# Optimization experiments

Measured on AMD Instinct MI355X. Metric: run time of the kernel, lower is better.

## Reference

```python
import jax, jax.numpy as jnp
import numpy as np

EPS = 1e-12  # matches torch F.normalize eps


def _l2_normalize(x, axis):
    n = jnp.sqrt(jnp.sum(x * x, axis=axis, keepdims=True))
    return x / jnp.maximum(n, EPS)


def setup_inputs() -> dict:
    key = jax.random.key(0)
    k1, k2 = jax.random.split(key)
    phi = jax.random.normal(k1, (64, 512), dtype=jnp.float32)          # (m, H)
    psi = jax.random.normal(k2, (64, 1024, 512), dtype=jnp.float32)    # (m, n, W)
    return {"phi": phi, "psi": psi}


def reference(phi, psi):
    phi = phi.astype(jnp.float32)
    psi = psi.astype(jnp.float32)
    m, H = phi.shape
    m2, n, W = psi.shape
    phi = _l2_normalize(phi, axis=1)   # rows of phi
    psi = _l2_normalize(psi, axis=2)   # each measurement vector

    g_phi_sq = jnp.square(phi @ phi.T)  # (m, m)

    # b[i, j] = sum_{u,v} (psi[i,u] . psi[j,v])^2 = ||psi_i psi_j^T||_F^2
    #         = <psi_i^T psi_i, psi_j^T psi_j>_F  (exact identity, avoids (m,m,n,n))
    S = jnp.einsum('inw,inv->iwv', psi, psi)   # (m, W, W) per-block Gram
    b = jnp.einsum('iwv,jwv->ij', S, S)        # (m, m)

    loss = jnp.sum(g_phi_sq * b) - jnp.float32(m * n)
    return loss
```

## Files before the change

kernel.cpp:

```cpp
#include <hip/hip_runtime.h>
#include <hip/hip_bf16.h>

typedef unsigned short u16;
typedef unsigned int u32;
typedef __attribute__((ext_vector_type(8))) short short8x;
typedef __attribute__((ext_vector_type(4))) float f32x4;

__device__ __forceinline__ u16 bf16u(float x) {
    __hip_bfloat16 h = __float2bfloat16(x);
    return *reinterpret_cast<u16*>(&h);
}

__device__ __forceinline__ void gload_lds16(const void* g, void* l) {
    __builtin_amdgcn_global_load_lds(
        (const __attribute__((address_space(1))) u32*)g,
        (__attribute__((address_space(3))) u32*)l, 16, 0, 0);
}

#define M_  64
#define N_  1024
#define W_  512
#define SP_ROW 163840

__global__ __launch_bounds__(256) void psinorm_t(const float* __restrict__ psi,
                                                 u16* __restrict__ psiT) {
    const int i  = blockIdx.y;
    const int nb = blockIdx.x;
    const int t  = threadIdx.x;
    const float* base = psi + ((size_t)i * N_ + (size_t)nb * 64) * W_;

    __shared__ float red[256];
    __shared__ float invs[64];
    __shared__ u32   tile[64][257];

    const int r = t >> 2, p = t & 3;
    const float4* rb = (const float4*)(base + r * W_ + p * 4);

    float4 v[32];
    float s = 0.f;
#pragma unroll
    for (int k = 0; k < 32; ++k) {
        v[k] = rb[k * 4];
        s += v[k].x * v[k].x + v[k].y * v[k].y + v[k].z * v[k].z + v[k].w * v[k].w;
    }
    red[t] = s;
    __syncthreads();
    if (t < 64) {
        float ss = red[4 * t] + red[4 * t + 1] + red[4 * t + 2] + red[4 * t + 3];
        invs[t] = 1.0f / fmaxf(sqrtf(ss), 1e-12f);
    }
    __syncthreads();

    {
        const float inv = invs[r];
#pragma unroll
        for (int k = 0; k < 32; ++k) {
            u32 p0 = (u32)bf16u(v[k].x * inv) | ((u32)bf16u(v[k].y * inv) << 16);
            u32 p1 = (u32)bf16u(v[k].z * inv) | ((u32)bf16u(v[k].w * inv) << 16);
            int wh = p * 2 + k * 8;
            tile[r][wh]     = p0;
            tile[r][wh + 1] = p1;
        }
    }
    __syncthreads();

    {
        const u16* t16 = (const u16*)&tile[0][0];
        int wv = t >> 6, lane = t & 63;
        size_t obase = (size_t)i * W_ * N_ + (size_t)nb * 64 + lane;
#pragma unroll 4
        for (int it = 0; it < 128; ++it) {
            int w = it * 4 + wv;
            psiT[obase + (size_t)w * N_] = t16[lane * 514 + w];
        }
    }
}

__global__ __launch_bounds__(256) void syrk_bf16(const u16* __restrict__ psiT,
                                                 u16* __restrict__ Sp) {
    const int L = blockIdx.x;
    const int q = L >> 3;
    const int i  = (L & 7) * 8 + q / 10;
    const int bt = q % 10;
    int tr, tc;
    if      (bt < 4) { tr = 0; tc = bt;     }
    else if (bt < 7) { tr = 1; tc = bt - 3; }
    else if (bt < 9) { tr = 2; tc = bt - 5; }
    else             { tr = 3; tc = 3;      }
    const int t = threadIdx.x;

    const u16* Abase = psiT + (size_t)i * W_ * N_ + (size_t)tr * 128 * N_;
    const u16* Bbase = psiT + (size_t)i * W_ * N_ + (size_t)tc * 128 * N_;

    __shared__ u16 ldsA[128][64];
    __shared__ u16 ldsB[128][64];

    const int lane = t & 63, wv = t >> 6;
    const int wr = wv >> 1, wc = wv & 1;
    const int lrow = lane & 15, lk8 = lane >> 4;

    f32x4 acc[4][4];
#pragma unroll
    for (int a = 0; a < 4; ++a)
#pragma unroll
        for (int b = 0; b < 4; ++b) acc[a][b] = (f32x4){0.f, 0.f, 0.f, 0.f};

    for (int kt = 0; kt < 16; ++kt) {
        const int k0 = kt * 64;
        __syncthreads();
#pragma unroll
        for (int r = 0; r < 4; ++r) {
            int c = r * 256 + t;
            int row = c >> 3, cch = c & 7;
            int scch = cch ^ (row & 7);
            gload_lds16(Abase + (size_t)row * N_ + k0 + scch * 8, &ldsA[row][cch * 8]);
            gload_lds16(Bbase + (size_t)row * N_ + k0 + scch * 8, &ldsB[row][cch * 8]);
        }
        __syncthreads();

#pragma unroll
        for (int ks = 0; ks < 2; ++ks) {
            short8x af[4], bf[4];
#pragma unroll
            for (int mf = 0; mf < 4; ++mf) {
                int row = wr * 64 + mf * 16 + lrow;
                int ch = (ks * 4 + lk8) ^ (row & 7);
                af[mf] = *(const short8x*)&ldsA[row][ch * 8];
            }
#pragma unroll
            for (int nf = 0; nf < 4; ++nf) {
                int row = wc * 64 + nf * 16 + lrow;
                int ch = (ks * 4 + lk8) ^ (row & 7);
                bf[nf] = *(const short8x*)&ldsB[row][ch * 8];
            }
#pragma unroll
            for (int mf = 0; mf < 4; ++mf)
#pragma unroll
                for (int nf = 0; nf < 4; ++nf)
                    acc[mf][nf] = __builtin_amdgcn_mfma_f32_16x16x32_bf16(
                        af[mf], bf[nf], acc[mf][nf], 0, 0, 0);
        }
    }

    const float sc = (tr == tc) ? 1.0f : 1.41421356237f;
    size_t Sbase = (size_t)i * SP_ROW + (size_t)bt * 16384;
#pragma unroll
    for (int mf = 0; mf < 4; ++mf)
#pragma unroll
        for (int nf = 0; nf < 4; ++nf)
#pragma unroll
            for (int reg = 0; reg < 4; ++reg) {
                int wl = wr * 64 + mf * 16 + lk8 * 4 + reg;
                int vl = wc * 64 + nf * 16 + lrow;
                Sp[Sbase + (size_t)wl * 128 + vl] = bf16u(acc[mf][nf][reg] * sc);
            }
}

__global__ __launch_bounds__(256) void bgemm(const u16* __restrict__ Sp,
                                             float* __restrict__ bp) {
    const int t = threadIdx.x;
    const int lane = t & 63, wv = t >> 6;
    const int wr = wv >> 1, wc = wv & 1;
    const int lrow = lane & 15, lk8 = lane >> 4;
    const size_t kc0 = (size_t)blockIdx.x * 256;

    f32x4 acc[2][2];
#pragma unroll
    for (int a = 0; a < 2; ++a)
#pragma unroll
        for (int b = 0; b < 2; ++b) acc[a][b] = (f32x4){0.f, 0.f, 0.f, 0.f};

#pragma unroll
    for (int ks = 0; ks < 8; ++ks) {
        short8x af[2], bf[2];
#pragma unroll
        for (int mf = 0; mf < 2; ++mf) {
            int row = wr * 32 + mf * 16 + lrow;
            af[mf] = *(const short8x*)(Sp + (size_t)row * SP_ROW + kc0 + (ks * 4 + lk8) * 8);
        }
#pragma unroll
        for (int nf = 0; nf < 2; ++nf) {
            int row = wc * 32 + nf * 16 + lrow;
            bf[nf] = *(const short8x*)(Sp + (size_t)row * SP_ROW + kc0 + (ks * 4 + lk8) * 8);
        }
#pragma unroll
        for (int mf = 0; mf < 2; ++mf)
#pragma unroll
            for (int nf = 0; nf < 2; ++nf)
                acc[mf][nf] = __builtin_amdgcn_mfma_f32_16x16x32_bf16(
                    af[mf], bf[nf], acc[mf][nf], 0, 0, 0);
    }

    float* out = bp + (size_t)blockIdx.x * 4096;
#pragma unroll
    for (int mf = 0; mf < 2; ++mf)
#pragma unroll
        for (int nf = 0; nf < 2; ++nf)
#pragma unroll
            for (int reg = 0; reg < 4; ++reg) {
                int ir = wr * 32 + mf * 16 + lk8 * 4 + reg;
                int jc = wc * 32 + nf * 16 + lrow;
                out[ir * 64 + jc] = acc[mf][nf][reg];
            }
}

__global__ __launch_bounds__(256) void bfinal(const float* __restrict__ bp,
                                              const float* __restrict__ phi,
                                              float* __restrict__ parts) {
    const int i = blockIdx.x, t = threadIdx.x;
    const int lane = t & 63, wv = t >> 6;

    __shared__ float red[256];
    __shared__ float brow[64];
    __shared__ float pi[512];
    __shared__ float dj[64], nsq[64];

    {
        float s = 0.f;
        for (int p = wv; p < 640; p += 4) s += bp[(size_t)p * 4096 + i * 64 + lane];
        red[t] = s;
    }
    pi[t] = phi[i * 512 + t];
    pi[t + 256] = phi[i * 512 + 256 + t];
    __syncthreads();
    if (t < 64) brow[t] = red[t] + red[64 + t] + red[128 + t] + red[192 + t];

    for (int jj = 0; jj < 16; ++jj) {
        int j = wv + jj * 4;
        const float* pj = phi + j * 512;
        float d = 0.f, nn = 0.f;
#pragma unroll
        for (int e = 0; e < 8; ++e) {
            float x = pj[lane + e * 64];
            d += pi[lane + e * 64] * x;
            nn += x * x;
        }
#pragma unroll
        for (int o = 32; o; o >>= 1) {
            d += __shfl_xor(d, o);
            nn += __shfl_xor(nn, o);
        }
        if (lane == 0) { dj[j] = d; nsq[j] = nn; }
    }
    __syncthreads();
    if (t < 64) {
        float ni = fmaxf(sqrtf(nsq[i]), 1e-12f);
        float nj = fmaxf(sqrtf(nsq[t]), 1e-12f);
        float g = dj[t] / (ni * nj);
        float val = g * g * brow[t];
#pragma unroll
        for (int o = 32; o; o >>= 1) val += __shfl_down(val, o);
        if (t == 0) parts[i] = val;
    }
}

__global__ void fsum(const float* __restrict__ parts, float* __restrict__ out) {
    const int t = threadIdx.x;
    float s = parts[t];
#pragma unroll
    for (int o = 32; o; o >>= 1) s += __shfl_down(s, o);
    if (t == 0) out[0] = s - 65536.0f;
}

__global__ void wsfail(float* __restrict__ out) {
    if (threadIdx.x == 0) out[0] = 1.0e30f;
}

extern "C" void kernel_launch(void* const* d_in, const int* in_sizes, int n_in,
                              void* d_out, int out_size, void* d_ws, size_t ws_size,
                              hipStream_t stream) {
    const float* phi = (const float*)d_in[0];
    const float* psi = (const float*)d_in[1];
    float* out = (float*)d_out;
    char* ws = (char*)d_ws;

    const size_t NEEDED = 67108864ull + 20971520ull + 256ull;
    if (ws_size < NEEDED) {
        wsfail<<<1, 64, 0, stream>>>(out);
        return;
    }
    u16*   psiT  = (u16*)(ws);
    float* bp    = (float*)(ws);
    u16*   Sp    = (u16*)(ws + 67108864);
    float* parts = (float*)(ws + 88080384);

    psinorm_t<<<dim3(16, 64), 256, 0, stream>>>(psi, psiT);
    syrk_bf16<<<640,          256, 0, stream>>>(psiT, Sp);
    bgemm    <<<640,          256, 0, stream>>>(Sp, bp);
    bfinal   <<<64,           256, 0, stream>>>(bp, phi, parts);
    fsum     <<<1,            64,  0, stream>>>(parts, out);
}
```

Baseline: 308.2 us.

## Double-buffer syrk LDS staging and coalesce psi normalize/transpose kernel

```diff
diff --git a/kernel.cpp b/kernel.cpp
--- a/kernel.cpp
+++ b/kernel.cpp
@@ -29,35 +29,29 @@
     const int t  = threadIdx.x;
     const float* base = psi + ((size_t)i * N_ + (size_t)nb * 64) * W_;
 
-    __shared__ float red[256];
-    __shared__ float invs[64];
-    __shared__ u32   tile[64][257];
-
-    const int r = t >> 2, p = t & 3;
-    const float4* rb = (const float4*)(base + r * W_ + p * 4);
-
-    float4 v[32];
-    float s = 0.f;
-#pragma unroll
-    for (int k = 0; k < 32; ++k) {
-        v[k] = rb[k * 4];
-        s += v[k].x * v[k].x + v[k].y * v[k].y + v[k].z * v[k].z + v[k].w * v[k].w;
-    }
-    red[t] = s;
-    __syncthreads();
-    if (t < 64) {
-        float ss = red[4 * t] + red[4 * t + 1] + red[4 * t + 2] + red[4 * t + 3];
-        invs[t] = 1.0f / fmaxf(sqrtf(ss), 1e-12f);
-    }
-    __syncthreads();
-
-    {
-        const float inv = invs[r];
-#pragma unroll
-        for (int k = 0; k < 32; ++k) {
+    __shared__ u32 tile[64][257];
+
+    const int sub = t & 15;
+
+#pragma unroll
+    for (int pp = 0; pp < 4; ++pp) {
+        const int r = pp * 16 + (t >> 4);
+        const float4* rb = (const float4*)(base + (size_t)r * W_) + sub;
+        float4 v[8];
+        float s = 0.f;
+#pragma unroll
+        for (int k = 0; k < 8; ++k) {
+            v[k] = rb[k * 16];
+            s += v[k].x * v[k].x + v[k].y * v[k].y + v[k].z * v[k].z + v[k].w * v[k].w;
+        }
+#pragma unroll
+        for (int o = 1; o < 16; o <<= 1) s += __shfl_xor(s, o);
+        const float inv = 1.0f / fmaxf(sqrtf(s), 1e-12f);
+#pragma unroll
+        for (int k = 0; k < 8; ++k) {
             u32 p0 = (u32)bf16u(v[k].x * inv) | ((u32)bf16u(v[k].y * inv) << 16);
             u32 p1 = (u32)bf16u(v[k].z * inv) | ((u32)bf16u(v[k].w * inv) << 16);
-            int wh = p * 2 + k * 8;
+            const int wh = sub * 2 + k * 32;
             tile[r][wh]     = p0;
             tile[r][wh + 1] = p1;
         }
@@ -66,12 +60,16 @@
 
     {
         const u16* t16 = (const u16*)&tile[0][0];
-        int wv = t >> 6, lane = t & 63;
-        size_t obase = (size_t)i * W_ * N_ + (size_t)nb * 64 + lane;
+        const int lane = t & 63, wv = t >> 6;
+        const int q  = lane & 31;
+        const int l5 = lane >> 5;
+        u32* out32 = (u32*)psiT + (size_t)i * (W_ * N_ / 2) + nb * 32;
 #pragma unroll 4
-        for (int it = 0; it < 128; ++it) {
-            int w = it * 4 + wv;
-            psiT[obase + (size_t)w * N_] = t16[lane * 514 + w];
+        for (int it = 0; it < 64; ++it) {
+            const int w = it * 8 + wv * 2 + l5;
+            u32 lo = (u32)t16[(2 * q)     * 514 + w];
+            u32 hi = (u32)t16[(2 * q + 1) * 514 + w];
+            out32[(size_t)w * 512 + q] = lo | (hi << 16);
         }
     }
 }
@@ -92,32 +90,38 @@
     const u16* Abase = psiT + (size_t)i * W_ * N_ + (size_t)tr * 128 * N_;
     const u16* Bbase = psiT + (size_t)i * W_ * N_ + (size_t)tc * 128 * N_;
 
-    __shared__ u16 ldsA[128][64];
-    __shared__ u16 ldsB[128][64];
+    __shared__ alignas(16) u16 ldsA[2][128][64];
+    __shared__ alignas(16) u16 ldsB[2][128][64];
 
     const int lane = t & 63, wv = t >> 6;
     const int wr = wv >> 1, wc = wv & 1;
     const int lrow = lane & 15, lk8 = lane >> 4;
 
-    f32x4 acc[4][4];
-#pragma unroll
-    for (int a = 0; a < 4; ++a)
-#pragma unroll
-        for (int b = 0; b < 4; ++b) acc[a][b] = (f32x4){0.f, 0.f, 0.f, 0.f};
-
-    for (int kt = 0; kt < 16; ++kt) {
+    auto STAGE = [&](int buf, int kt) {
         const int k0 = kt * 64;
-        __syncthreads();
 #pragma unroll
         for (int r = 0; r < 4; ++r) {
             int c = r * 256 + t;
             int row = c >> 3, cch = c & 7;
             int scch = cch ^ (row & 7);
-            gload_lds16(Abase + (size_t)row * N_ + k0 + scch * 8, &ldsA[row][cch * 8]);
-            gload_lds16(Bbase + (size_t)row * N_ + k0 + scch * 8, &ldsB[row][cch * 8]);
-        }
-        __syncthreads();
-
+            gload_lds16(Abase + (size_t)row * N_ + k0 + scch * 8, &ldsA[buf][row][cch * 8]);
+            gload_lds16(Bbase + (size_t)row * N_ + k0 + scch * 8, &ldsB[buf][row][cch * 8]);
+        }
+    };
+
+    f32x4 acc[4][4];
+#pragma unroll
+    for (int a = 0; a < 4; ++a)
+#pragma unroll
+        for (int b = 0; b < 4; ++b) acc[a][b] = (f32x4){0.f, 0.f, 0.f, 0.f};
+
+    STAGE(0, 0);
+    asm volatile("s_waitcnt vmcnt(0)" ::: "memory");
+    __builtin_amdgcn_s_barrier();
+
+    int cur = 0;
+    for (int kt = 0; kt < 16; ++kt) {
+        if (kt < 15) STAGE(cur ^ 1, kt + 1);
 #pragma unroll
         for (int ks = 0; ks < 2; ++ks) {
             short8x af[4], bf[4];
@@ -125,13 +129,13 @@
             for (int mf = 0; mf < 4; ++mf) {
                 int row = wr * 64 + mf * 16 + lrow;
                 int ch = (ks * 4 + lk8) ^ (row & 7);
-                af[mf] = *(const short8x*)&ldsA[row][ch * 8];
+                af[mf] = *(const short8x*)&ldsA[cur][row][ch * 8];
             }
 #pragma unroll
             for (int nf = 0; nf < 4; ++nf) {
                 int row = wc * 64 + nf * 16 + lrow;
                 int ch = (ks * 4 + lk8) ^ (row & 7);
-                bf[nf] = *(const short8x*)&ldsB[row][ch * 8];
+                bf[nf] = *(const short8x*)&ldsB[cur][row][ch * 8];
             }
 #pragma unroll
             for (int mf = 0; mf < 4; ++mf)
@@ -140,6 +144,10 @@
                     acc[mf][nf] = __builtin_amdgcn_mfma_f32_16x16x32_bf16(
                         af[mf], bf[nf], acc[mf][nf], 0, 0, 0);
         }
+        asm volatile("s_waitcnt vmcnt(0)" ::: "memory");
+        __builtin_amdgcn_sched_barrier(0);
+        __builtin_amdgcn_s_barrier();
+        cur ^= 1;
     }
 
     const float sc = (tr == tc) ? 1.0f : 1.41421356237f;
```

After: 311.5 us. Within noise of the previous version (+1.1%).
